# Kernel optimization log

Measured on AMD Instinct MI355X. Metric: run time of the kernel, lower is better.

Reference implementation:

```python
import jax, jax.numpy as jnp
import numpy as np

BETA = 0.99      # rootfind_module beta
TOL = 1e-3       # torch loop: while V(fx*a) - t > 0.001
MAX_ITER = 50    # safety cap (torch loop is uncapped but converges)


def _fhat(x, W1, b1, W2, b2):
    # x: (B,1,D) -> (B,1,D)
    h = jnp.tanh(x @ W1 + b1)
    return h @ W2 + b2


def _V_sample(z, Wv1, Wv2):
    # z: (1,D) -> scalar Lyapunov value
    h = jnp.tanh(z @ Wv1)
    y = h @ Wv2
    return jnp.sum(y * y) + 0.01 * jnp.sum(z * z)


def _V(z, Wv1, Wv2):
    # z: (B,1,D) -> (B,1,1)
    h = jnp.tanh(z @ Wv1)
    y = h @ Wv2
    v = jnp.sum(y * y, axis=(-2, -1)) + 0.01 * jnp.sum(z * z, axis=(-2, -1))
    return v[:, None, None]


def _newton_step(fhatx, target, alpha, Wv1, Wv2):
    # newton_iter.forward: F = alpha - (V(fhatx*alpha) - target) / dV/dalpha
    z = fhatx * alpha                                  # (B,1,D)
    Vz = _V(z, Wv1, Wv2)                               # (B,1,1)
    gradV = jax.vmap(jax.grad(_V_sample), in_axes=(0, None, None))(z, Wv1, Wv2)
    dV_da = jnp.sum(gradV * fhatx, axis=(-2, -1))[:, None, None]
    return alpha - (Vz - target) / dV_da


def _rootfind(fhatx, target, Wv1, Wv2):
    # batched, masked replacement of torch per-sample Python while loops
    B = fhatx.shape[0]
    alpha0 = jnp.ones((B, 1, 1), fhatx.dtype)

    def cond(carry):
        i, alpha = carry
        resid = _V(fhatx * alpha, Wv1, Wv2) - target
        return jnp.logical_and(i < MAX_ITER, jnp.any(resid > TOL))

    def body(carry):
        i, alpha = carry
        resid = _V(fhatx * alpha, Wv1, Wv2) - target
        new_alpha = _newton_step(fhatx, target, alpha, Wv1, Wv2)
        alpha = jnp.where(resid > TOL, new_alpha, alpha)  # only unconverged samples move
        return (i + 1, alpha)

    _, alpha = jax.lax.while_loop(cond, body, (jnp.int32(0), alpha0))
    return alpha


def setup_inputs() -> dict:
    key = jax.random.key(0)
    ks = jax.random.split(key, 5)
    B, D, H, HV, VO = 8192, 512, 2048, 512, 256
    s = 0.02
    return {
        "x": jax.random.normal(ks[0], (B, 1, D), jnp.float32),
        "W1": jax.random.normal(ks[1], (D, H), jnp.float32) * s,
        "b1": jnp.zeros((H,), jnp.float32),
        "W2": jax.random.normal(ks[2], (H, D), jnp.float32) * s,
        "b2": jnp.zeros((D,), jnp.float32),
        "Wv1": jax.random.normal(ks[3], (D, HV), jnp.float32) * s,
        "Wv2": jax.random.normal(ks[4], (HV, VO), jnp.float32) * s,
    }


def reference(x, W1, b1, W2, b2, Wv1, Wv2):
    fhatx = _fhat(x, W1, b1, W2, b2)        # (B,1,D)
    target = BETA * _V(x, Wv1, Wv2)         # (B,1,1)
    alpha = _rootfind(fhatx, target, Wv1, Wv2)
    return fhatx * alpha                    # x_root, (B,1,D)
```

## Files before the change

### kernel.cpp

```cpp
#include <hip/hip_runtime.h>
#include <hip/hip_bf16.h>
#include <stdint.h>
#include <stddef.h>

typedef __bf16 bf16_t;
typedef __bf16 bf16x8 __attribute__((ext_vector_type(8)));
typedef __bf16 bf16x4 __attribute__((ext_vector_type(4)));
typedef float  f32x4  __attribute__((ext_vector_type(4)));

#define NB 8192
#define ND 512
#define NH 2048
#define NHV 512
#define NVO 256
#define RF_TOL 1e-3f
#define NEWTON_MAX 16

typedef const __attribute__((address_space(1))) void gvoid_t;
typedef __attribute__((address_space(3))) void lvoid_t;

__device__ __forceinline__ void gload_lds16(const void* g, void* l) {
  __builtin_amdgcn_global_load_lds((gvoid_t*)g, (lvoid_t*)l, 16, 0, 0);
}

__device__ __forceinline__ float fast_tanhf(float x) {
  x = fminf(fmaxf(x, -15.0f), 15.0f);
  float e = __expf(2.0f * x);
  return (e - 1.0f) * __builtin_amdgcn_rcpf(e + 1.0f);
}

struct GJob {
  const bf16_t* A;
  const bf16_t* Bt;
  const float*  bias;
  bf16_t* Cbf;
  float*  Cf;
  float*  rowsq;
  int N, K, nbx, tanh_act;
};

__device__ __forceinline__ void tr_body(const float* __restrict__ src, bf16_t* __restrict__ dst,
                                        int R, int C, int bidx, float (*tile)[33]) {
  const int tilesx = C >> 5;
  const int bi = (bidx / tilesx) << 5, bj = (bidx % tilesx) << 5;
  const int t = threadIdx.x, tx = t & 31, ty = t >> 5;
#pragma unroll
  for (int r = ty; r < 32; r += 8)
    tile[r][tx] = src[(size_t)(bi + r) * C + (bj + tx)];
  __syncthreads();
#pragma unroll
  for (int r = ty; r < 32; r += 8)
    dst[(size_t)(bj + r) * R + (bi + tx)] = (bf16_t)tile[tx][r];
}

template<int BM, bool SWZ, int TBX>
__global__ __launch_bounds__(256, 4)
void gemm_kernel(GJob j0, GJob j1,
                 const float* tw2, bf16_t* tw2t, const float* twv2, bf16_t* twv2t)
{
  constexpr int MI = BM / 32;
  __shared__ bf16_t As[BM * 64];
  __shared__ bf16_t Bs[128 * 64];

  int bx0, by;
  if (SWZ) {
    int f = (int)blockIdx.y * (int)gridDim.x + (int)blockIdx.x;
    const int nwg = (int)gridDim.x * (int)gridDim.y;
    f = (f & 7) * (nwg >> 3) + (f >> 3);
    bx0 = f % (int)gridDim.x;
    by  = f / (int)gridDim.x;
  } else {
    bx0 = (int)blockIdx.x;
    by  = (int)blockIdx.y;
  }

  if (TBX > 0 && bx0 >= TBX) {
    float (*tile)[33] = reinterpret_cast<float(*)[33]>(As);
    const int idx = (bx0 - TBX) * (int)gridDim.y + by;
    if (idx < 1024) tr_body(tw2, tw2t, 2048, 512, idx, tile);
    else            tr_body(twv2, twv2t, 512, 256, idx - 1024, tile);
    return;
  }

  const bool first = bx0 < j0.nbx;
  const GJob jb = first ? j0 : j1;
  const int bx = bx0 - (first ? 0 : j0.nbx);
  const int K = jb.K, N = jb.N;

  const int t = threadIdx.x, lane = t & 63, w = t >> 6;
  const int wm = w >> 1, wn = w & 1;
  const int la = lane & 15, lg = lane >> 4;
  const size_t m0 = (size_t)by * BM, n0 = (size_t)bx * 128;

  size_t soffA[MI], soffB[4]; int doff[4];
#pragma unroll
  for (int j = 0; j < 4; ++j) {
    const int off = t * 16 + j * 4096;
    const int r = off >> 7, c = off & 127;
    const size_t so = (size_t)r * K + ((c ^ ((r & 7) << 4)) >> 1);
    if (j < MI) soffA[j] = so;
    soffB[j] = so;
    doff[j] = off;
  }
  const bf16_t* Ab = jb.A + m0 * K;
  const bf16_t* Bb = jb.Bt + n0 * K;

  int abyte[MI][2], bbyte[4][2];
#pragma unroll
  for (int ks = 0; ks < 2; ++ks) {
#pragma unroll
    for (int i = 0; i < MI; ++i) {
      const int ra = wm * (BM / 2) + i * 16 + la;
      abyte[i][ks] = ra * 128 + ((ks * 64 + lg * 16) ^ ((ra & 7) << 4));
    }
#pragma unroll
    for (int j = 0; j < 4; ++j) {
      const int rb = wn * 64 + j * 16 + la;
      bbyte[j][ks] = rb * 128 + ((ks * 64 + lg * 16) ^ ((rb & 7) << 4));
    }
  }

  f32x4 acc[MI][4] = {};
  const int nsteps = K >> 6;

  for (int ts = 0; ts < nsteps; ++ts) {
    const int k0 = ts << 6;
#pragma unroll
    for (int j = 0; j < MI; ++j)
      gload_lds16(Ab + soffA[j] + k0, (char*)As + doff[j]);
#pragma unroll
    for (int j = 0; j < 4; ++j)
      gload_lds16(Bb + soffB[j] + k0, (char*)Bs + doff[j]);
    __syncthreads();

    bf16x8 afr[MI][2], bfr[4][2];
#pragma unroll
    for (int ks = 0; ks < 2; ++ks) {
#pragma unroll
      for (int i = 0; i < MI; ++i)
        afr[i][ks] = *(const bf16x8*)((const char*)As + abyte[i][ks]);
#pragma unroll
      for (int j = 0; j < 4; ++j)
        bfr[j][ks] = *(const bf16x8*)((const char*)Bs + bbyte[j][ks]);
    }
#pragma unroll
    for (int ks = 0; ks < 2; ++ks)
#pragma unroll
      for (int i = 0; i < MI; ++i)
#pragma unroll
        for (int j = 0; j < 4; ++j)
          acc[i][j] = __builtin_amdgcn_mfma_f32_16x16x32_bf16(afr[i][ks], bfr[j][ks], acc[i][j], 0, 0, 0);
    __syncthreads();
  }

  if (jb.rowsq) {
#pragma unroll
    for (int i = 0; i < MI; ++i) {
#pragma unroll
      for (int r = 0; r < 4; ++r) {
        float s = 0.0f;
#pragma unroll
        for (int j = 0; j < 4; ++j) { float v = acc[i][j][r]; s = fmaf(v, v, s); }
        s += __shfl_xor(s, 1); s += __shfl_xor(s, 2);
        s += __shfl_xor(s, 4); s += __shfl_xor(s, 8);
        if (la == 0)
          atomicAdd(&jb.rowsq[m0 + wm * (BM / 2) + i * 16 + lg * 4 + r], s);
      }
    }
    return;
  }
#pragma unroll
  for (int i = 0; i < MI; ++i) {
#pragma unroll
    for (int j = 0; j < 4; ++j) {
      const size_t col = n0 + wn * 64 + j * 16 + la;
      const float bv = jb.bias ? jb.bias[col] : 0.0f;
#pragma unroll
      for (int r = 0; r < 4; ++r) {
        const size_t row = m0 + wm * (BM / 2) + i * 16 + lg * 4 + r;
        float v = acc[i][j][r] + bv;
        if (jb.tanh_act) v = fast_tanhf(v);
        if (jb.Cbf) jb.Cbf[row * N + col] = (bf16_t)v;
        if (jb.Cf)  jb.Cf [row * N + col] = v;
      }
    }
  }
}

__global__ void prep_kernel(const float* __restrict__ x, bf16_t* __restrict__ xbf, float* __restrict__ xsq,
                            const float* __restrict__ W1, bf16_t* __restrict__ w1t,
                            const float* __restrict__ Wv1, bf16_t* __restrict__ wv1t,
                            float* __restrict__ yxsq)
{
  __shared__ float tile[32][33];
  const int b = blockIdx.x;
  if (b < 1024)      tr_body(W1, w1t, 512, 2048, b, tile);
  else if (b < 1280) tr_body(Wv1, wv1t, 512, 512, b - 1024, tile);
  else {
    const int t = threadIdx.x;
    const int row = (b - 1280) * 4 + (t >> 6), l = t & 63;
    const float4* sr = (const float4*)(x + (size_t)row * ND);
    bf16x4* dw = (bf16x4*)(xbf + (size_t)row * ND);
    float s = 0.0f;
#pragma unroll
    for (int c = l; c < ND / 4; c += 64) {
      float4 v = sr[c];
      s = fmaf(v.x, v.x, fmaf(v.y, v.y, fmaf(v.z, v.z, fmaf(v.w, v.w, s))));
      bf16x4 o;
      o[0] = (bf16_t)v.x; o[1] = (bf16_t)v.y; o[2] = (bf16_t)v.z; o[3] = (bf16_t)v.w;
      dw[c] = o;
    }
#pragma unroll
    for (int m = 32; m; m >>= 1) s += __shfl_xor(s, m);
    if (l == 0) xsq[row] = s;
    if (l == 1) yxsq[row] = 0.0f;
  }
}

__global__ __launch_bounds__(512, 1)
void newton_kernel(const bf16_t* __restrict__ fbf, const bf16_t* __restrict__ wv1t,
                   const bf16_t* __restrict__ Wv2t,
                   const float* __restrict__ yxsq, const float* __restrict__ xsq,
                   float* __restrict__ out)
{
  __shared__ alignas(16) bf16_t hs[32 * 512];
  __shared__ alignas(16) bf16_t es[32 * 512];
  __shared__ float red[8][32][2];
  __shared__ float alpha_s[32], fsq_s[32], tgt_s[32];
  __shared__ int notdone_s;

  const int t = threadIdx.x, lane = t & 63, w = t >> 6;
  const int la = lane & 15, lg = lane >> 4;
  const int s_base = blockIdx.x * 32;
  const int arow = lane & 31, ahi = lane >> 5;

  {
    const int row = t >> 4, c0 = (t & 15) * 4;
    float s = 0.0f;
#pragma unroll
    for (int i = 0; i < 4; ++i) {
      const int k8 = c0 + i;
      bf16x8 v = *(const bf16x8*)(fbf + (size_t)(s_base + row) * ND + k8 * 8);
#pragma unroll
      for (int q = 0; q < 8; ++q) { float f = (float)v[q]; s = fmaf(f, f, s); }
      *(bf16x8*)((char*)hs + (row << 10) + ((k8 ^ (row & 7)) << 4)) = v;
    }
    s += __shfl_xor(s, 1); s += __shfl_xor(s, 2); s += __shfl_xor(s, 4); s += __shfl_xor(s, 8);
    if ((t & 15) == 0) fsq_s[row] = s;
  }
  if (t < 32) {
    alpha_s[t] = 1.0f;
    tgt_s[t] = 0.99f * (yxsq[s_base + t] + 0.01f * xsq[s_base + t]);
  }
  __syncthreads();

  f32x4 uacc[2][4] = {};
#pragma unroll
  for (int k = 0; k < 16; ++k) {
    bf16x8 afr[2];
#pragma unroll
    for (int mt = 0; mt < 2; ++mt) {
      const int row = mt * 16 + la;
      afr[mt] = *(const bf16x8*)((const char*)hs + (row << 10) + (((k * 4 + lg) ^ (row & 7)) << 4));
    }
#pragma unroll
    for (int nt = 0; nt < 4; ++nt) {
      const bf16x8 b = *(const bf16x8*)(wv1t + (size_t)(w * 64 + nt * 16 + la) * ND + k * 32 + lg * 8);
#pragma unroll
      for (int mt = 0; mt < 2; ++mt)
        uacc[mt][nt] = __builtin_amdgcn_mfma_f32_16x16x32_bf16(afr[mt], b, uacc[mt][nt], 0, 0, 0);
    }
  }

#pragma unroll
  for (int mt = 0; mt < 2; ++mt)
#pragma unroll
    for (int nt = 0; nt < 4; ++nt)
#pragma unroll
      for (int r = 0; r < 4; ++r) {
        const int row = mt * 16 + lg * 4 + r;
        const int col = w * 64 + nt * 16 + la;
        *(bf16_t*)((char*)es + (row << 10) + (((col >> 3) ^ (row & 7)) << 4) + (col & 7) * 2)
            = (bf16_t)uacc[mt][nt][r];
      }
  __syncthreads();

  bf16x8 ureg[4];
#pragma unroll
  for (int i = 0; i < 4; ++i) {
    const int k8 = w * 8 + ahi * 4 + i;
    ureg[i] = *(const bf16x8*)((const char*)es + (arow << 10) + ((k8 ^ (arow & 7)) << 4));
  }

  bf16x8 bfr[2][16];
#pragma unroll
  for (int nt = 0; nt < 2; ++nt) {
    const bf16_t* bp = Wv2t + (size_t)(w * 32 + nt * 16 + la) * NHV + lg * 8;
#pragma unroll
    for (int k = 0; k < 16; ++k)
      bfr[nt][k] = *(const bf16x8*)(bp + k * 32);
  }
  __syncthreads();

  for (int it = 0; it < NEWTON_MAX; ++it) {
    {
      const float c2 = 2.0f * alpha_s[arow];
#pragma unroll
      for (int i = 0; i < 4; ++i) {
        const int k8 = w * 8 + ahi * 4 + i;
        const int byte = (arow << 10) + ((k8 ^ (arow & 7)) << 4);
        bf16x8 uv = ureg[i], hf, ef;
#pragma unroll
        for (int q = 0; q < 8; ++q) {
          float u = (float)uv[q];
          float e = __expf(c2 * u);
          float h = (e - 1.0f) * __builtin_amdgcn_rcpf(e + 1.0f);
          hf[q] = (bf16_t)h;
          ef[q] = (bf16_t)(u * (1.0f - h * h));
        }
        *(bf16x8*)((char*)hs + byte) = hf;
        *(bf16x8*)((char*)es + byte) = ef;
      }
    }
    __syncthreads();

    f32x4 accy[2][2] = {};
    f32x4 accw[2][2] = {};
#pragma unroll
    for (int k = 0; k < 16; ++k) {
#pragma unroll
      for (int mt = 0; mt < 2; ++mt) {
        const int row = mt * 16 + la;
        const int byte = (row << 10) + (((k * 4 + lg) ^ (row & 7)) << 4);
        bf16x8 hf = *(const bf16x8*)((const char*)hs + byte);
        bf16x8 ef = *(const bf16x8*)((const char*)es + byte);
#pragma unroll
        for (int nt = 0; nt < 2; ++nt) {
          accy[mt][nt] = __builtin_amdgcn_mfma_f32_16x16x32_bf16(hf, bfr[nt][k], accy[mt][nt], 0, 0, 0);
          accw[mt][nt] = __builtin_amdgcn_mfma_f32_16x16x32_bf16(ef, bfr[nt][k], accw[mt][nt], 0, 0, 0);
        }
      }
    }

#pragma unroll
    for (int mt = 0; mt < 2; ++mt) {
#pragma unroll
      for (int r = 0; r < 4; ++r) {
        float sy = 0.0f, sw = 0.0f;
#pragma unroll
        for (int nt = 0; nt < 2; ++nt) {
          float yv = accy[mt][nt][r], wv = accw[mt][nt][r];
          sy = fmaf(yv, yv, sy);
          sw = fmaf(yv, wv, sw);
        }
        sy += __shfl_xor(sy, 1); sw += __shfl_xor(sw, 1);
        sy += __shfl_xor(sy, 2); sw += __shfl_xor(sw, 2);
        sy += __shfl_xor(sy, 4); sw += __shfl_xor(sw, 4);
        sy += __shfl_xor(sy, 8); sw += __shfl_xor(sw, 8);
        if (la == 0) {
          red[w][mt * 16 + lg * 4 + r][0] = sy;
          red[w][mt * 16 + lg * 4 + r][1] = sw;
        }
      }
    }
    __syncthreads();
    if (t < 32) {
      float SY = 0.0f, SW = 0.0f;
#pragma unroll
      for (int w8 = 0; w8 < 8; ++w8) {
        SY += red[w8][t][0];
        SW += red[w8][t][1];
      }
      float a = alpha_s[t];
      const float fs = fsq_s[t];
      const float V = SY + 0.01f * a * a * fs;
      const float dV = 2.0f * SW + 0.02f * a * fs;
      const float resid = V - tgt_s[t];
      const bool go = resid > RF_TOL;
      if (go) {
        if (it == 0)
          alpha_s[t] = __builtin_sqrtf(tgt_s[t] / V);
        else
          alpha_s[t] = a - resid / dV;
      }
      const int nd = __any(go);
      if (t == 0) notdone_s = nd;
    }
    __syncthreads();
    if (!notdone_s) break;
  }

  {
    const int r = t >> 4;
    const int c4 = t & 15;
    const float a = alpha_s[r];
    if (a != 1.0f) {
      const size_t rb = (size_t)(s_base + r) * ND;
      float4* dp = (float4*)(out + rb);
#pragma unroll
      for (int jj = 0; jj < 8; ++jj) {
        float4 v = dp[c4 + jj * 16];
        v.x *= a; v.y *= a; v.z *= a; v.w *= a;
        dp[c4 + jj * 16] = v;
      }
    }
  }
}

extern "C" void kernel_launch(void* const* d_in, const int* in_sizes, int n_in,
                              void* d_out, int out_size, void* d_ws, size_t ws_size,
                              hipStream_t stream)
{
  (void)in_sizes; (void)n_in; (void)out_size; (void)ws_size;
  const float* x   = (const float*)d_in[0];
  const float* W1  = (const float*)d_in[1];
  const float* b1  = (const float*)d_in[2];
  const float* W2  = (const float*)d_in[3];
  const float* b2  = (const float*)d_in[4];
  const float* Wv1 = (const float*)d_in[5];
  const float* Wv2 = (const float*)d_in[6];
  float* out = (float*)d_out;

  char* ws = (char*)d_ws;
  size_t off = 0;
  auto alloc = [&](size_t n) { char* p = ws + off; off += (n + 255) & ~(size_t)255; return p; };

  bf16_t* xbf  = (bf16_t*)alloc((size_t)NB * ND * 2);
  bf16_t* w1t  = (bf16_t*)alloc((size_t)NH * ND * 2);
  bf16_t* w2t  = (bf16_t*)alloc((size_t)ND * NH * 2);
  bf16_t* wv1t = (bf16_t*)alloc((size_t)NHV * ND * 2);
  bf16_t* wv2t = (bf16_t*)alloc((size_t)NVO * NHV * 2);
  bf16_t* h1   = (bf16_t*)alloc((size_t)NB * NH * 2);
  bf16_t* fbf  = (bf16_t*)alloc((size_t)NB * ND * 2);
  bf16_t* hx   = (bf16_t*)alloc((size_t)NB * NHV * 2);
  float*  xsq  = (float*)alloc((size_t)NB * 4);
  float*  yxsq = (float*)alloc((size_t)NB * 4);

  prep_kernel<<<3328, 256, 0, stream>>>(x, xbf, xsq, W1, w1t, Wv1, wv1t, yxsq);

  GJob jh1 { xbf, w1t,  b1,      h1,  nullptr, nullptr, NH,  ND, NH  / 128, 1 };
  GJob jhx { xbf, wv1t, nullptr, hx,  nullptr, nullptr, NHV, ND, NHV / 128, 1 };
  gemm_kernel<128, true, 20><<<dim3(38, NB / 128), 256, 0, stream>>>(jh1, jhx, W2, w2t, Wv2, wv2t);

  GJob jf  { h1,  w2t,  b2,      fbf, out,     nullptr, ND,  NH, ND  / 128, 0 };
  GJob jy  { hx,  wv2t, nullptr, nullptr, nullptr, yxsq, NVO, NHV, NVO / 128, 0 };
  gemm_kernel<64, true, 0><<<dim3(ND / 128 + NVO / 128, NB / 64), 256, 0, stream>>>(jf, jy, nullptr, nullptr, nullptr, nullptr);

  newton_kernel<<<NB / 32, 512, 0, stream>>>(fbf, wv1t, wv2t, yxsq, xsq, out);
}
```

Before: 111.0 us.

## Fuse target V(x) second-layer GEMM into Newton kernel, drop atomic rowsq path

Moves the hx @ Wv2 product and its row sum-of-squares, which give the target V(x), out of the second GEMM launch and into the start of the Newton kernel. The Wv2 fragments the Newton kernel already preloads are reused, and the result is reduced through shared memory instead of global atomics. This removes the yxsq buffer, its zero-init in prep, and the extra grid columns in the second GEMM. The cost is a longer Newton-kernel prologue, since it now loads hx and runs an extra MFMA pass per block, and the Wv2 register fragments stay live across that prologue.

```diff
diff --git a/kernel.cpp b/kernel.cpp
--- a/kernel.cpp
+++ b/kernel.cpp
@@ -35,7 +35,6 @@
   const float*  bias;
   bf16_t* Cbf;
   float*  Cf;
-  float*  rowsq;
   int N, K, nbx, tanh_act;
 };
 
@@ -153,22 +152,6 @@
     __syncthreads();
   }
 
-  if (jb.rowsq) {
-#pragma unroll
-    for (int i = 0; i < MI; ++i) {
-#pragma unroll
-      for (int r = 0; r < 4; ++r) {
-        float s = 0.0f;
-#pragma unroll
-        for (int j = 0; j < 4; ++j) { float v = acc[i][j][r]; s = fmaf(v, v, s); }
-        s += __shfl_xor(s, 1); s += __shfl_xor(s, 2);
-        s += __shfl_xor(s, 4); s += __shfl_xor(s, 8);
-        if (la == 0)
-          atomicAdd(&jb.rowsq[m0 + wm * (BM / 2) + i * 16 + lg * 4 + r], s);
-      }
-    }
-    return;
-  }
 #pragma unroll
   for (int i = 0; i < MI; ++i) {
 #pragma unroll
@@ -189,8 +172,7 @@
 
 __global__ void prep_kernel(const float* __restrict__ x, bf16_t* __restrict__ xbf, float* __restrict__ xsq,
                             const float* __restrict__ W1, bf16_t* __restrict__ w1t,
-                            const float* __restrict__ Wv1, bf16_t* __restrict__ wv1t,
-                            float* __restrict__ yxsq)
+                            const float* __restrict__ Wv1, bf16_t* __restrict__ wv1t)
 {
   __shared__ float tile[32][33];
   const int b = blockIdx.x;
@@ -213,15 +195,13 @@
 #pragma unroll
     for (int m = 32; m; m >>= 1) s += __shfl_xor(s, m);
     if (l == 0) xsq[row] = s;
-    if (l == 1) yxsq[row] = 0.0f;
   }
 }
 
 __global__ __launch_bounds__(512, 1)
-void newton_kernel(const bf16_t* __restrict__ fbf, const bf16_t* __restrict__ wv1t,
-                   const bf16_t* __restrict__ Wv2t,
-                   const float* __restrict__ yxsq, const float* __restrict__ xsq,
-                   float* __restrict__ out)
+void newton_kernel(const bf16_t* __restrict__ fbf, const bf16_t* __restrict__ hx,
+                   const bf16_t* __restrict__ wv1t, const bf16_t* __restrict__ Wv2t,
+                   const float* __restrict__ xsq, float* __restrict__ out)
 {
   __shared__ alignas(16) bf16_t hs[32 * 512];
   __shared__ alignas(16) bf16_t es[32 * 512];
@@ -234,6 +214,59 @@
   const int s_base = blockIdx.x * 32;
   const int arow = lane & 31, ahi = lane >> 5;
 
+  bf16x8 bfr[2][16];
+#pragma unroll
+  for (int nt = 0; nt < 2; ++nt) {
+    const bf16_t* bp = Wv2t + (size_t)(w * 32 + nt * 16 + la) * NHV + lg * 8;
+#pragma unroll
+    for (int k = 0; k < 16; ++k)
+      bfr[nt][k] = *(const bf16x8*)(bp + k * 32);
+  }
+
+  {
+    const int row = t >> 4, c0 = (t & 15) * 4;
+#pragma unroll
+    for (int i = 0; i < 4; ++i) {
+      const int k8 = c0 + i;
+      bf16x8 v = *(const bf16x8*)(hx + (size_t)(s_base + row) * NHV + k8 * 8);
+      *(bf16x8*)((char*)hs + (row << 10) + ((k8 ^ (row & 7)) << 4)) = v;
+    }
+  }
+  __syncthreads();
+  {
+    f32x4 accy[2][2] = {};
+#pragma unroll
+    for (int k = 0; k < 16; ++k)
+#pragma unroll
+      for (int mt = 0; mt < 2; ++mt) {
+        const int row = mt * 16 + la;
+        const int byte = (row << 10) + (((k * 4 + lg) ^ (row & 7)) << 4);
+        bf16x8 hf = *(const bf16x8*)((const char*)hs + byte);
+#pragma unroll
+        for (int nt = 0; nt < 2; ++nt)
+          accy[mt][nt] = __builtin_amdgcn_mfma_f32_16x16x32_bf16(hf, bfr[nt][k], accy[mt][nt], 0, 0, 0);
+      }
+#pragma unroll
+    for (int mt = 0; mt < 2; ++mt)
+#pragma unroll
+      for (int r = 0; r < 4; ++r) {
+        float sy = 0.0f;
+#pragma unroll
+        for (int nt = 0; nt < 2; ++nt) { float yv = accy[mt][nt][r]; sy = fmaf(yv, yv, sy); }
+        sy += __shfl_xor(sy, 1); sy += __shfl_xor(sy, 2);
+        sy += __shfl_xor(sy, 4); sy += __shfl_xor(sy, 8);
+        if (la == 0) red[w][mt * 16 + lg * 4 + r][0] = sy;
+      }
+  }
+  __syncthreads();
+  if (t < 32) {
+    float SY = 0.0f;
+#pragma unroll
+    for (int w8 = 0; w8 < 8; ++w8) SY += red[w8][t][0];
+    tgt_s[t] = 0.99f * (SY + 0.01f * xsq[s_base + t]);
+    alpha_s[t] = 1.0f;
+  }
+
   {
     const int row = t >> 4, c0 = (t & 15) * 4;
     float s = 0.0f;
@@ -247,10 +280,6 @@
     }
     s += __shfl_xor(s, 1); s += __shfl_xor(s, 2); s += __shfl_xor(s, 4); s += __shfl_xor(s, 8);
     if ((t & 15) == 0) fsq_s[row] = s;
-  }
-  if (t < 32) {
-    alpha_s[t] = 1.0f;
-    tgt_s[t] = 0.99f * (yxsq[s_base + t] + 0.01f * xsq[s_base + t]);
   }
   __syncthreads();
 
@@ -290,15 +319,6 @@
   for (int i = 0; i < 4; ++i) {
     const int k8 = w * 8 + ahi * 4 + i;
     ureg[i] = *(const bf16x8*)((const char*)es + (arow << 10) + ((k8 ^ (arow & 7)) << 4));
-  }
-
-  bf16x8 bfr[2][16];
-#pragma unroll
-  for (int nt = 0; nt < 2; ++nt) {
-    const bf16_t* bp = Wv2t + (size_t)(w * 32 + nt * 16 + la) * NHV + lg * 8;
-#pragma unroll
-    for (int k = 0; k < 16; ++k)
-      bfr[nt][k] = *(const bf16x8*)(bp + k * 32);
   }
   __syncthreads();
 
@@ -434,17 +454,15 @@
   bf16_t* fbf  = (bf16_t*)alloc((size_t)NB * ND * 2);
   bf16_t* hx   = (bf16_t*)alloc((size_t)NB * NHV * 2);
   float*  xsq  = (float*)alloc((size_t)NB * 4);
-  float*  yxsq = (float*)alloc((size_t)NB * 4);
-
-  prep_kernel<<<3328, 256, 0, stream>>>(x, xbf, xsq, W1, w1t, Wv1, wv1t, yxsq);
-
-  GJob jh1 { xbf, w1t,  b1,      h1,  nullptr, nullptr, NH,  ND, NH  / 128, 1 };
-  GJob jhx { xbf, wv1t, nullptr, hx,  nullptr, nullptr, NHV, ND, NHV / 128, 1 };
+
+  prep_kernel<<<3328, 256, 0, stream>>>(x, xbf, xsq, W1, w1t, Wv1, wv1t);
+
+  GJob jh1 { xbf, w1t,  b1,      h1,  nullptr, NH,  ND, NH  / 128, 1 };
+  GJob jhx { xbf, wv1t, nullptr, hx,  nullptr, NHV, ND, NHV / 128, 1 };
   gemm_kernel<128, true, 20><<<dim3(38, NB / 128), 256, 0, stream>>>(jh1, jhx, W2, w2t, Wv2, wv2t);
 
-  GJob jf  { h1,  w2t,  b2,      fbf, out,     nullptr, ND,  NH, ND  / 128, 0 };
-  GJob jy  { hx,  wv2t, nullptr, nullptr, nullptr, yxsq, NVO, NHV, NVO / 128, 0 };
-  gemm_kernel<64, true, 0><<<dim3(ND / 128 + NVO / 128, NB / 64), 256, 0, stream>>>(jf, jy, nullptr, nullptr, nullptr, nullptr);
-
-  newton_kernel<<<NB / 32, 512, 0, stream>>>(fbf, wv1t, wv2t, yxsq, xsq, out);
-}
+  GJob jf  { h1,  w2t,  b2,      fbf, out,     ND,  NH, ND / 128, 0 };
+  gemm_kernel<64, true, 0><<<dim3(ND / 128, NB / 64), 256, 0, stream>>>(jf, jf, nullptr, nullptr, nullptr, nullptr);
+
+  newton_kernel<<<NB / 32, 512, 0, stream>>>(fbf, hx, wv1t, wv2t, xsq, out);
+}
```

Measured after the change: 115.8 us. 4.4% more time.
